# Optimization experiments

Hardware: AMD Instinct MI355X
Metric: run time of the kernel (lower is better)

The kernel has to match this reference:

```python
import jax, jax.numpy as jnp
import numpy as np

N = 100000      # nodes
E = 1600000     # edges
D_IN = 256
D_HID = 256
D_OUT = 256
DROP_P = 0.5


def setup_inputs() -> dict:
    key = jax.random.key(0)
    ks = jax.random.split(key, 10)
    s = 1.0 / np.sqrt(D_HID)
    return {
        "z": jax.random.normal(ks[0], (N, D_OUT), jnp.float32),
        "omega": jax.random.normal(ks[1], (N, D_IN), jnp.float32),
        "edge_index": jax.random.randint(ks[2], (2, E), 0, N, jnp.int32),
        "W_lin": jax.random.normal(ks[3], (D_IN, D_HID), jnp.float32) * s,
        "b_lin": jnp.zeros((D_HID,), jnp.float32),
        "W_g1": jax.random.normal(ks[4], (D_HID, D_HID), jnp.float32) * s,
        "b_g1": jnp.zeros((D_HID,), jnp.float32),
        "W_g2": jax.random.normal(ks[5], (D_HID, D_OUT), jnp.float32) * s,
        "b_g2": jnp.zeros((D_OUT,), jnp.float32),
        "mask1": jax.random.bernoulli(ks[6], 1.0 - DROP_P, (N, D_HID)),
        "mask2": jax.random.bernoulli(ks[7], 1.0 - DROP_P, (N, D_HID)),
    }


def _gcn_norm(edge_index):
    # add self-loops, symmetric normalization deg^-1/2 * deg^-1/2
    loop = jnp.arange(N, dtype=edge_index.dtype)
    src = jnp.concatenate([edge_index[0], loop])
    dst = jnp.concatenate([edge_index[1], loop])
    deg = jax.ops.segment_sum(jnp.ones_like(dst, jnp.float32), dst, num_segments=N)
    dinv = jax.lax.rsqrt(deg)  # deg >= 1 because of self-loops
    norm = dinv[src] * dinv[dst]  # [E+N]
    return src, dst, norm


def _gcn_conv(x, W, b, src, dst, norm):
    h = x @ W                                  # [N, d_out]
    msg = h[src] * norm[:, None]               # gather over edges
    out = jax.ops.segment_sum(msg, dst, num_segments=N)  # scatter-add
    return out + b


def _dropout(x, mask):
    return jnp.where(mask, x * (1.0 / (1.0 - DROP_P)), 0.0)


def reference(z, omega, edge_index, W_lin, b_lin, W_g1, b_g1, W_g2, b_g2, mask1, mask2):
    src, dst, norm = _gcn_norm(edge_index)
    # layer 0: Linear + relu + dropout
    h = _dropout(jax.nn.relu(omega @ W_lin + b_lin), mask1)
    # layer 1: GCNConv + relu + dropout
    h = _dropout(jax.nn.relu(_gcn_conv(h, W_g1, b_g1, src, dst, norm)), mask2)
    # layer 2: GCNConv
    h = _gcn_conv(h, W_g2, b_g2, src, dst, norm)
    return z * h
```

## Files before the change

### kernel.cpp

```cpp
#include <hip/hip_runtime.h>
#include <stdint.h>

#define NN 100000
#define EE 1600000
#define DD 256

typedef __bf16 bf16;
typedef __attribute__((ext_vector_type(8))) __bf16 bf16x8;
typedef __attribute__((ext_vector_type(4))) float f32x4;
typedef __attribute__((ext_vector_type(4))) unsigned int u32x4;
typedef __attribute__((ext_vector_type(8))) unsigned short u16x8;

typedef __attribute__((address_space(1))) const unsigned int g_u32c;
typedef __attribute__((address_space(3))) unsigned int lds_u32;

__device__ __forceinline__ float bflo(unsigned int u) {
    union { unsigned int u; float f; } x; x.u = u << 16; return x.f;
}
__device__ __forceinline__ float bfhi(unsigned int u) {
    union { unsigned int u; float f; } x; x.u = u & 0xFFFF0000u; return x.f;
}
__device__ __forceinline__ unsigned short f2bf(float f) {
    return __builtin_bit_cast(unsigned short, (__bf16)f);
}

#define NSUB 128
__global__ __launch_bounds__(256) void count_deg_k(
    const int* __restrict__ dst, int* __restrict__ cnt) {
    int bid = blockIdx.x;
    int prt = bid & 7;
    int sub = bid >> 3;
    int lo = prt * (NN >> 3);
    int hi = (prt == 7) ? NN : lo + (NN >> 3);
    const int per = EE / NSUB;
    int e0 = sub * per;
    int e1 = (sub == NSUB - 1) ? EE : e0 + per;
    for (int e = e0 + threadIdx.x; e < e1; e += 256) {
        int d = dst[e];
        if (d >= lo && d < hi) atomicAdd(&cnt[d], 1);
    }
}
__global__ __launch_bounds__(256) void scan_blk_k(const int* __restrict__ cnt,
                                                  int* __restrict__ part,
                                                  int* __restrict__ bsum,
                                                  float* __restrict__ dinv) {
    __shared__ int buf[256];
    int i = blockIdx.x * 256 + threadIdx.x;
    int v = 0;
    if (i < NN) { v = cnt[i] + 1; dinv[i] = rsqrtf((float)v); }
    buf[threadIdx.x] = v;
    __syncthreads();
    for (int off = 1; off < 256; off <<= 1) {
        int t = (threadIdx.x >= off) ? buf[threadIdx.x - off] : 0;
        __syncthreads();
        buf[threadIdx.x] += t;
        __syncthreads();
    }
    if (i < NN) part[i] = buf[threadIdx.x];
    if (threadIdx.x == 255) bsum[blockIdx.x] = buf[255];
}
__global__ __launch_bounds__(512) void scan_top_k(const int* __restrict__ bsum,
                                                  int* __restrict__ bpre, int nb) {
    __shared__ int buf[512];
    int v = (threadIdx.x < (unsigned)nb) ? bsum[threadIdx.x] : 0;
    buf[threadIdx.x] = v;
    __syncthreads();
    for (int off = 1; off < 512; off <<= 1) {
        int t = (threadIdx.x >= off) ? buf[threadIdx.x - off] : 0;
        __syncthreads();
        buf[threadIdx.x] += t;
        __syncthreads();
    }
    if (threadIdx.x < (unsigned)nb) bpre[threadIdx.x] = buf[threadIdx.x] - v;
}
__global__ void scan_fin_k(const int* __restrict__ part, const int* __restrict__ bpre,
                           const int* __restrict__ cnt,
                           int* __restrict__ offs, int* __restrict__ cur,
                           int* __restrict__ cs) {
    int i = blockIdx.x * 256 + threadIdx.x;
    if (i >= NN) return;
    int o1 = part[i] + bpre[blockIdx.x];
    offs[i + 1] = o1;
    if (i == 0) offs[0] = 0;
    int o = o1 - (cnt[i] + 1);
    cs[o] = i;
    cur[i] = o + 1;
}
__global__ __launch_bounds__(256) void fill_csr_k(
    const int* __restrict__ src, const int* __restrict__ dst,
    int* __restrict__ cur, int* __restrict__ cs) {
    int bid = blockIdx.x;
    int prt = bid & 7;
    int sub = bid >> 3;
    int lo = prt * (NN >> 3);
    int hi = (prt == 7) ? NN : lo + (NN >> 3);
    const int per = EE / NSUB;
    int e0 = sub * per;
    int e1 = (sub == NSUB - 1) ? EE : e0 + per;
    for (int e = e0 + threadIdx.x; e < e1; e += 256) {
        int d = dst[e];
        if (d >= lo && d < hi) {
            int s = src[e];
            int pos = atomicAdd(&cur[d], 1);
            cs[pos] = s;
        }
    }
}

__global__ __launch_bounds__(256) void prep_k(
    const float* __restrict__ W0, const float* __restrict__ W1, const float* __restrict__ W2,
    bf16* __restrict__ T0, bf16* __restrict__ T1, bf16* __restrict__ T2,
    const unsigned int* __restrict__ m, int* __restrict__ flag) {
    int b = blockIdx.x;
    if (b == 192) {
        if (threadIdx.x < 64) {
            unsigned int v = m[threadIdx.x];
            int bad = (v > 1u && v != 0x3F800000u) ? 1 : 0;
            unsigned long long bl = __ballot(bad);
            if (threadIdx.x == 0) *flag = (bl != 0ull) ? 1 : 0;
        }
        return;
    }
    const float* W = b < 64 ? W0 : (b < 128 ? W1 : W2);
    bf16*       T  = b < 64 ? T0 : (b < 128 ? T1 : T2);
    int bb = b & 63;
    __shared__ float tile[32][33];
    int bx = bb & 7, by = bb >> 3;
    int tx = threadIdx.x & 31, ty = threadIdx.x >> 5;
    #pragma unroll
    for (int r = 0; r < 32; r += 8)
        tile[ty + r][tx] = W[(size_t)(by * 32 + ty + r) * DD + bx * 32 + tx];
    __syncthreads();
    #pragma unroll
    for (int r = 0; r < 32; r += 8)
        T[(size_t)(bx * 32 + ty + r) * DD + by * 32 + tx] = (bf16)tile[tx][ty + r];
}

template <int ID, int EPI, int F32A>
__global__ __launch_bounds__(256) void gemm_k(
    const void* __restrict__ Ap, const bf16* __restrict__ Wt,
    const float* __restrict__ bias, const void* __restrict__ mask,
    const int* __restrict__ flagp, const float* __restrict__ z,
    const float* __restrict__ dinv, void* __restrict__ outp) {
    __shared__ __align__(16) bf16 As[64 * 64];
    __shared__ __align__(16) bf16 Bs[256 * 64];

    int m0 = blockIdx.x * 64;
    if (m0 >= NN) return;
    int tid = threadIdx.x;
    int wid = tid >> 6, lane = tid & 63;
    int lr = lane & 15, lk = lane >> 4;

    f32x4 acc[4][4] = {};

    for (int k0 = 0; k0 < DD; k0 += 64) {
        #pragma unroll
        for (int i = 0; i < 2; i++) {
            int f = i * 256 + tid;
            int row = f >> 3;
            int c   = (f & 7) * 8;
            int gr = m0 + row; if (gr > NN - 1) gr = NN - 1;
            if (F32A) {
                const float* sp = (const float*)Ap + (size_t)gr * DD + k0 + c;
                float4 v0 = *(const float4*)sp;
                float4 v1 = *(const float4*)(sp + 4);
                u16x8 o = { f2bf(v0.x), f2bf(v0.y), f2bf(v0.z), f2bf(v0.w),
                            f2bf(v1.x), f2bf(v1.y), f2bf(v1.z), f2bf(v1.w) };
                *(u16x8*)(As + row * 64 + c) = o;
            } else {
                __builtin_amdgcn_global_load_lds(
                    (g_u32c*)((const bf16*)Ap + (size_t)gr * DD + k0 + c),
                    (lds_u32*)(As + (size_t)f * 8), 16, 0, 0);
            }
        }
        #pragma unroll
        for (int i = 0; i < 8; i++) {
            int f = i * 256 + tid;
            int row = f >> 3;
            int c   = (f & 7) * 8;
            __builtin_amdgcn_global_load_lds(
                (g_u32c*)(Wt + (size_t)row * DD + k0 + c),
                (lds_u32*)(Bs + (size_t)f * 8), 16, 0, 0);
        }
        __syncthreads();
        #pragma unroll
        for (int kk = 0; kk < 2; kk++) {
            bf16x8 af[4], bfr[4];
            #pragma unroll
            for (int mi = 0; mi < 4; mi++)
                af[mi] = *(const bf16x8*)(As + (mi * 16 + lr) * 64 + kk * 32 + lk * 8);
            #pragma unroll
            for (int ni = 0; ni < 4; ni++)
                bfr[ni] = *(const bf16x8*)(Bs + (wid * 64 + ni * 16 + lr) * 64 + kk * 32 + lk * 8);
            #pragma unroll
            for (int mi = 0; mi < 4; mi++)
                #pragma unroll
                for (int ni = 0; ni < 4; ni++)
                    acc[mi][ni] = __builtin_amdgcn_mfma_f32_16x16x32_bf16(
                        bfr[ni], af[mi], acc[mi][ni], 0, 0, 0);
        }
        __syncthreads();
    }

    int bm = (EPI == 1) ? *flagp : 0;
    #pragma unroll
    for (int mi = 0; mi < 4; mi++) {
        int gr = m0 + mi * 16 + lr;
        if (gr >= NN) continue;
        float ds = (EPI == 1) ? dinv[gr] : 0.f;
        #pragma unroll
        for (int ni = 0; ni < 4; ni++) {
            int gc = wid * 64 + ni * 16 + lk * 4;
            size_t idx = (size_t)gr * DD + gc;
            float4 b4 = *(const float4*)(bias + gc);
            float v0 = acc[mi][ni][0] + b4.x;
            float v1 = acc[mi][ni][1] + b4.y;
            float v2 = acc[mi][ni][2] + b4.z;
            float v3 = acc[mi][ni][3] + b4.w;
            if (EPI == 1) {
                v0 = fmaxf(v0, 0.f); v1 = fmaxf(v1, 0.f);
                v2 = fmaxf(v2, 0.f); v3 = fmaxf(v3, 0.f);
                if (bm) {
                    uchar4 u = *(const uchar4*)((const unsigned char*)mask + idx);
                    v0 *= u.x ? 2.f : 0.f; v1 *= u.y ? 2.f : 0.f;
                    v2 *= u.z ? 2.f : 0.f; v3 *= u.w ? 2.f : 0.f;
                } else {
                    uint4 u = *(const uint4*)((const unsigned int*)mask + idx);
                    v0 *= u.x ? 2.f : 0.f; v1 *= u.y ? 2.f : 0.f;
                    v2 *= u.z ? 2.f : 0.f; v3 *= u.w ? 2.f : 0.f;
                }
                v0 *= ds; v1 *= ds; v2 *= ds; v3 *= ds;
                ushort4 o = { f2bf(v0), f2bf(v1), f2bf(v2), f2bf(v3) };
                *(ushort4*)((unsigned short*)outp + idx) = o;
            } else {
                f32x4 zz = __builtin_nontemporal_load((const f32x4*)(z + idx));
                f32x4 o = { v0 * zz.x, v1 * zz.y, v2 * zz.z, v3 * zz.w };
                __builtin_nontemporal_store(o, (f32x4*)((float*)outp + idx));
            }
        }
    }
}

#define AGG_GET(J, UVAR, MVAR)                                                   \
    {                                                                            \
        int _i = 2 * (J) + half;                                                 \
        int _s = __shfl(sl, _i & 63);                                            \
        MVAR = (_i < nume) ? 1.f : 0.f;                                          \
        UVAR = *(const u32x4*)(tb + (((size_t)(unsigned)_s) << 9) + lcoff);      \
    }
#define AGG_FMA(UVAR, MVAR)                                                      \
    {                                                                            \
        acc[0] = fmaf(MVAR, bflo(UVAR.x), acc[0]);                               \
        acc[1] = fmaf(MVAR, bfhi(UVAR.x), acc[1]);                               \
        acc[2] = fmaf(MVAR, bflo(UVAR.y), acc[2]);                               \
        acc[3] = fmaf(MVAR, bfhi(UVAR.y), acc[3]);                               \
        acc[4] = fmaf(MVAR, bflo(UVAR.z), acc[4]);                               \
        acc[5] = fmaf(MVAR, bfhi(UVAR.z), acc[5]);                               \
        acc[6] = fmaf(MVAR, bflo(UVAR.w), acc[6]);                               \
        acc[7] = fmaf(MVAR, bfhi(UVAR.w), acc[7]);                               \
    }

__global__ __launch_bounds__(256) void agg_k(
    const bf16* __restrict__ t, const int* __restrict__ offs,
    const int* __restrict__ cs, const float* __restrict__ dinv,
    bf16* __restrict__ out) {
    int node = blockIdx.x * 4 + (threadIdx.x >> 6);
    if (node >= NN) return;
    int lane = threadIdx.x & 63;
    int half = lane >> 5;
    int lc = lane & 31;
    int beg = offs[node], end = offs[node + 1];

    float acc[8] = {};
    const char* tb = (const char*)t;
    size_t lcoff = (size_t)(lc << 4);

    for (int base = beg; base < end; base += 64) {
        int nume = min(64, end - base);
        int sl = 0;
        if (lane < nume) sl = __builtin_nontemporal_load(cs + base + lane);
        int nit = (nume + 1) >> 1;

        u32x4 ua, ub, uc, ud;
        float ma, mb, mc, md;
        AGG_GET(0, ua, ma);
        AGG_GET(1, ub, mb);
        AGG_GET(2, uc, mc);
        int j = 0;
        for (; j + 3 < nit; j += 4) {
            AGG_GET(j + 3, ud, md); AGG_FMA(ua, ma);
            AGG_GET(j + 4, ua, ma); AGG_FMA(ub, mb);
            AGG_GET(j + 5, ub, mb); AGG_FMA(uc, mc);
            AGG_GET(j + 6, uc, mc); AGG_FMA(ud, md);
        }
        int rem = nit - j;
        if (rem > 0) AGG_FMA(ua, ma);
        if (rem > 1) AGG_FMA(ub, mb);
        if (rem > 2) AGG_FMA(uc, mc);
    }

    float dn = dinv[node];
    #pragma unroll
    for (int i = 0; i < 8; i++) {
        acc[i] += __shfl_xor(acc[i], 32);
        acc[i] *= dn;
    }
    if (half == 0) {
        u16x8 o = { f2bf(acc[0]), f2bf(acc[1]), f2bf(acc[2]), f2bf(acc[3]),
                    f2bf(acc[4]), f2bf(acc[5]), f2bf(acc[6]), f2bf(acc[7]) };
        __builtin_nontemporal_store(o, (u16x8*)((unsigned short*)out + (size_t)node * DD + lc * 8));
    }
}

extern "C" void kernel_launch(void* const* d_in, const int* in_sizes, int n_in,
                              void* d_out, int out_size, void* d_ws, size_t ws_size,
                              hipStream_t stream) {
    const float* z     = (const float*)d_in[0];
    const float* omega = (const float*)d_in[1];
    const int*   eidx  = (const int*)d_in[2];
    const float* W_lin = (const float*)d_in[3];
    const float* b_lin = (const float*)d_in[4];
    const float* W_g1  = (const float*)d_in[5];
    const float* b_g1  = (const float*)d_in[6];
    const float* W_g2  = (const float*)d_in[7];
    const float* b_g2  = (const float*)d_in[8];
    const void*  mask1 = d_in[9];
    const void*  mask2 = d_in[10];

    const int* e_src = eidx;
    const int* e_dst = eidx + EE;

    char* p = (char*)d_ws;
    size_t off = 0;
    auto alloc = [&](size_t bytes) -> char* {
        char* r = p + off;
        off = (off + bytes + 255) & ~(size_t)255;
        return r;
    };
    const int NB256 = (NN + 255) / 256;
    int*   flag = (int*)  alloc(4);
    int*   cnt  = (int*)  alloc((size_t)NN * 4);
    int*   offs = (int*)  alloc(((size_t)NN + 1) * 4);
    int*   cur  = (int*)  alloc((size_t)NN * 4);
    int*   part = (int*)  alloc((size_t)NN * 4);
    int*   bsum = (int*)  alloc(512 * 4);
    int*   bpre = (int*)  alloc(512 * 4);
    float* dinv = (float*)alloc((size_t)NN * 4);
    int*   cs   = (int*)  alloc((size_t)(EE + NN) * 4);
    bf16*  WtL  = (bf16*) alloc((size_t)DD * DD * 2);
    bf16*  Wt1  = (bf16*) alloc((size_t)DD * DD * 2);
    bf16*  Wt2  = (bf16*) alloc((size_t)DD * DD * 2);
    const size_t NBH = (size_t)NN * DD * 2;
    bf16*  S1   = (bf16*) alloc(NBH);
    bf16*  S2   = (bf16*) alloc(NBH);

    (void)hipMemsetAsync(cnt, 0, (size_t)NN * 4, stream);
    count_deg_k<<<NSUB * 8, 256, 0, stream>>>(e_dst, cnt);
    scan_blk_k <<<NB256, 256, 0, stream>>>(cnt, part, bsum, dinv);
    scan_top_k <<<1, 512, 0, stream>>>(bsum, bpre, NB256);
    scan_fin_k <<<NB256, 256, 0, stream>>>(part, bpre, cnt, offs, cur, cs);
    fill_csr_k <<<NSUB * 8, 256, 0, stream>>>(e_src, e_dst, cur, cs);

    prep_k<<<193, 256, 0, stream>>>(W_lin, W_g1, W_g2, WtL, Wt1, Wt2,
                                    (const unsigned int*)mask1, flag);

    const int GB = (NN + 63) / 64;
    gemm_k<0, 1, 1><<<GB, 256, 0, stream>>>(omega, WtL, b_lin, mask1, flag, nullptr, dinv, S1);
    agg_k<<<NN / 4, 256, 0, stream>>>(S1, offs, cs, dinv, S2);
    gemm_k<1, 1, 0><<<GB, 256, 0, stream>>>(S2, Wt1, b_g1, mask2, flag, nullptr, dinv, S1);
    agg_k<<<NN / 4, 256, 0, stream>>>(S1, offs, cs, dinv, S2);
    gemm_k<2, 2, 0><<<GB, 256, 0, stream>>>(S2, Wt2, b_g2, nullptr, flag, z, dinv, d_out);
}
```

Baseline: 611.3 us.

## Fuse neighbor aggregation into the following GEMM via shared-memory tile

Merges the sparse aggregation kernel with the next dense GEMM. Each block aggregates 64 nodes into an LDS tile and multiplies it by the weight matrix in two 128-column halves. This removes the bf16 round trip of the aggregated activations through global memory and two kernel launches. In exchange, each block serializes 16 nodes per wave during aggregation, so it exposes fewer concurrent gathers. The larger LDS footprint may also reduce occupancy.

```diff
diff --git a/kernel.cpp b/kernel.cpp
--- a/kernel.cpp
+++ b/kernel.cpp
@@ -136,12 +136,40 @@
         T[(size_t)(bx * 32 + ty + r) * DD + by * 32 + tx] = (bf16)tile[tx][ty + r];
 }
 
-template <int ID, int EPI, int F32A>
-__global__ __launch_bounds__(256) void gemm_k(
-    const void* __restrict__ Ap, const bf16* __restrict__ Wt,
+template <int EPI>
+__device__ __forceinline__ void epilogue4(
+    float v0, float v1, float v2, float v3, size_t idx, int gc,
+    const float* __restrict__ bias, const void* __restrict__ mask, int bm,
+    const float* __restrict__ z, float ds, void* __restrict__ outp) {
+    float4 b4 = *(const float4*)(bias + gc);
+    v0 += b4.x; v1 += b4.y; v2 += b4.z; v3 += b4.w;
+    if (EPI == 1) {
+        v0 = fmaxf(v0, 0.f); v1 = fmaxf(v1, 0.f);
+        v2 = fmaxf(v2, 0.f); v3 = fmaxf(v3, 0.f);
+        if (bm) {
+            uchar4 u = *(const uchar4*)((const unsigned char*)mask + idx);
+            v0 *= u.x ? 2.f : 0.f; v1 *= u.y ? 2.f : 0.f;
+            v2 *= u.z ? 2.f : 0.f; v3 *= u.w ? 2.f : 0.f;
+        } else {
+            uint4 u = *(const uint4*)((const unsigned int*)mask + idx);
+            v0 *= u.x ? 2.f : 0.f; v1 *= u.y ? 2.f : 0.f;
+            v2 *= u.z ? 2.f : 0.f; v3 *= u.w ? 2.f : 0.f;
+        }
+        v0 *= ds; v1 *= ds; v2 *= ds; v3 *= ds;
+        ushort4 o = { f2bf(v0), f2bf(v1), f2bf(v2), f2bf(v3) };
+        *(ushort4*)((unsigned short*)outp + idx) = o;
+    } else {
+        f32x4 zz = __builtin_nontemporal_load((const f32x4*)(z + idx));
+        f32x4 o = { v0 * zz.x, v1 * zz.y, v2 * zz.z, v3 * zz.w };
+        __builtin_nontemporal_store(o, (f32x4*)((float*)outp + idx));
+    }
+}
+
+__global__ __launch_bounds__(256) void gemm0_k(
+    const float* __restrict__ Ap, const bf16* __restrict__ Wt,
     const float* __restrict__ bias, const void* __restrict__ mask,
-    const int* __restrict__ flagp, const float* __restrict__ z,
-    const float* __restrict__ dinv, void* __restrict__ outp) {
+    const int* __restrict__ flagp, const float* __restrict__ dinv,
+    bf16* __restrict__ outp) {
     __shared__ __align__(16) bf16 As[64 * 64];
     __shared__ __align__(16) bf16 Bs[256 * 64];
 
@@ -160,18 +188,12 @@
             int row = f >> 3;
             int c   = (f & 7) * 8;
             int gr = m0 + row; if (gr > NN - 1) gr = NN - 1;
-            if (F32A) {
-                const float* sp = (const float*)Ap + (size_t)gr * DD + k0 + c;
-                float4 v0 = *(const float4*)sp;
-                float4 v1 = *(const float4*)(sp + 4);
-                u16x8 o = { f2bf(v0.x), f2bf(v0.y), f2bf(v0.z), f2bf(v0.w),
-                            f2bf(v1.x), f2bf(v1.y), f2bf(v1.z), f2bf(v1.w) };
-                *(u16x8*)(As + row * 64 + c) = o;
-            } else {
-                __builtin_amdgcn_global_load_lds(
-                    (g_u32c*)((const bf16*)Ap + (size_t)gr * DD + k0 + c),
-                    (lds_u32*)(As + (size_t)f * 8), 16, 0, 0);
-            }
+            const float* sp = Ap + (size_t)gr * DD + k0 + c;
+            float4 v0 = *(const float4*)sp;
+            float4 v1 = *(const float4*)(sp + 4);
+            u16x8 o = { f2bf(v0.x), f2bf(v0.y), f2bf(v0.z), f2bf(v0.w),
+                        f2bf(v1.x), f2bf(v1.y), f2bf(v1.z), f2bf(v1.w) };
+            *(u16x8*)(As + row * 64 + c) = o;
         }
         #pragma unroll
         for (int i = 0; i < 8; i++) {
@@ -202,41 +224,18 @@
         __syncthreads();
     }
 
-    int bm = (EPI == 1) ? *flagp : 0;
+    int bm = *flagp;
     #pragma unroll
     for (int mi = 0; mi < 4; mi++) {
         int gr = m0 + mi * 16 + lr;
         if (gr >= NN) continue;
-        float ds = (EPI == 1) ? dinv[gr] : 0.f;
+        float ds = dinv[gr];
         #pragma unroll
         for (int ni = 0; ni < 4; ni++) {
             int gc = wid * 64 + ni * 16 + lk * 4;
             size_t idx = (size_t)gr * DD + gc;
-            float4 b4 = *(const float4*)(bias + gc);
-            float v0 = acc[mi][ni][0] + b4.x;
-            float v1 = acc[mi][ni][1] + b4.y;
-            float v2 = acc[mi][ni][2] + b4.z;
-            float v3 = acc[mi][ni][3] + b4.w;
-            if (EPI == 1) {
-                v0 = fmaxf(v0, 0.f); v1 = fmaxf(v1, 0.f);
-                v2 = fmaxf(v2, 0.f); v3 = fmaxf(v3, 0.f);
-                if (bm) {
-                    uchar4 u = *(const uchar4*)((const unsigned char*)mask + idx);
-                    v0 *= u.x ? 2.f : 0.f; v1 *= u.y ? 2.f : 0.f;
-                    v2 *= u.z ? 2.f : 0.f; v3 *= u.w ? 2.f : 0.f;
-                } else {
-                    uint4 u = *(const uint4*)((const unsigned int*)mask + idx);
-                    v0 *= u.x ? 2.f : 0.f; v1 *= u.y ? 2.f : 0.f;
-                    v2 *= u.z ? 2.f : 0.f; v3 *= u.w ? 2.f : 0.f;
-                }
-                v0 *= ds; v1 *= ds; v2 *= ds; v3 *= ds;
-                ushort4 o = { f2bf(v0), f2bf(v1), f2bf(v2), f2bf(v3) };
-                *(ushort4*)((unsigned short*)outp + idx) = o;
-            } else {
-                f32x4 zz = __builtin_nontemporal_load((const f32x4*)(z + idx));
-                f32x4 o = { v0 * zz.x, v1 * zz.y, v2 * zz.z, v3 * zz.w };
-                __builtin_nontemporal_store(o, (f32x4*)((float*)outp + idx));
-            }
+            epilogue4<1>(acc[mi][ni][0], acc[mi][ni][1], acc[mi][ni][2], acc[mi][ni][3],
+                         idx, gc, bias, mask, bm, nullptr, ds, outp);
         }
     }
 }
@@ -260,55 +259,111 @@
         acc[7] = fmaf(MVAR, bfhi(UVAR.w), acc[7]);                               \
     }
 
-__global__ __launch_bounds__(256) void agg_k(
-    const bf16* __restrict__ t, const int* __restrict__ offs,
+template <int ID, int EPI>
+__global__ __launch_bounds__(256) void aggemm_k(
+    const bf16* __restrict__ S, const int* __restrict__ offs,
     const int* __restrict__ cs, const float* __restrict__ dinv,
-    bf16* __restrict__ out) {
-    int node = blockIdx.x * 4 + (threadIdx.x >> 6);
-    if (node >= NN) return;
-    int lane = threadIdx.x & 63;
-    int half = lane >> 5;
-    int lc = lane & 31;
-    int beg = offs[node], end = offs[node + 1];
-
-    float acc[8] = {};
-    const char* tb = (const char*)t;
+    const bf16* __restrict__ Wt, const float* __restrict__ bias,
+    const void* __restrict__ mask, const int* __restrict__ flagp,
+    const float* __restrict__ z, void* __restrict__ outp) {
+    __shared__ __align__(16) bf16 Ag[64][264];
+    __shared__ __align__(16) bf16 Bs[128 * 64];
+
+    int m0 = blockIdx.x * 64;
+    int tid = threadIdx.x;
+    int wid = tid >> 6, lane = tid & 63;
+    int half = lane >> 5, lc = lane & 31;
+    int lr = lane & 15, lk = lane >> 4;
+    const char* tb = (const char*)S;
     size_t lcoff = (size_t)(lc << 4);
 
-    for (int base = beg; base < end; base += 64) {
-        int nume = min(64, end - base);
-        int sl = 0;
-        if (lane < nume) sl = __builtin_nontemporal_load(cs + base + lane);
-        int nit = (nume + 1) >> 1;
-
-        u32x4 ua, ub, uc, ud;
-        float ma, mb, mc, md;
-        AGG_GET(0, ua, ma);
-        AGG_GET(1, ub, mb);
-        AGG_GET(2, uc, mc);
-        int j = 0;
-        for (; j + 3 < nit; j += 4) {
-            AGG_GET(j + 3, ud, md); AGG_FMA(ua, ma);
-            AGG_GET(j + 4, ua, ma); AGG_FMA(ub, mb);
-            AGG_GET(j + 5, ub, mb); AGG_FMA(uc, mc);
-            AGG_GET(j + 6, uc, mc); AGG_FMA(ud, md);
-        }
-        int rem = nit - j;
-        if (rem > 0) AGG_FMA(ua, ma);
-        if (rem > 1) AGG_FMA(ub, mb);
-        if (rem > 2) AGG_FMA(uc, mc);
-    }
-
-    float dn = dinv[node];
+    for (int nn = 0; nn < 16; nn++) {
+        int node = m0 + wid * 16 + nn;
+        if (node >= NN) break;
+        int beg = offs[node], end = offs[node + 1];
+        float acc[8] = {};
+        for (int base = beg; base < end; base += 64) {
+            int nume = min(64, end - base);
+            int sl = 0;
+            if (lane < nume) sl = __builtin_nontemporal_load(cs + base + lane);
+            int nit = (nume + 1) >> 1;
+            u32x4 ua, ub, uc, ud;
+            float ma, mb, mc, md;
+            AGG_GET(0, ua, ma);
+            AGG_GET(1, ub, mb);
+            AGG_GET(2, uc, mc);
+            int j = 0;
+            for (; j + 3 < nit; j += 4) {
+                AGG_GET(j + 3, ud, md); AGG_FMA(ua, ma);
+                AGG_GET(j + 4, ua, ma); AGG_FMA(ub, mb);
+                AGG_GET(j + 5, ub, mb); AGG_FMA(uc, mc);
+                AGG_GET(j + 6, uc, mc); AGG_FMA(ud, md);
+            }
+            int rem = nit - j;
+            if (rem > 0) AGG_FMA(ua, ma);
+            if (rem > 1) AGG_FMA(ub, mb);
+            if (rem > 2) AGG_FMA(uc, mc);
+        }
+        float dn = dinv[node];
+        #pragma unroll
+        for (int i = 0; i < 8; i++) {
+            acc[i] += __shfl_xor(acc[i], 32);
+            acc[i] *= dn;
+        }
+        if (half == 0) {
+            u16x8 o = { f2bf(acc[0]), f2bf(acc[1]), f2bf(acc[2]), f2bf(acc[3]),
+                        f2bf(acc[4]), f2bf(acc[5]), f2bf(acc[6]), f2bf(acc[7]) };
+            *(u16x8*)(&Ag[wid * 16 + nn][lc * 8]) = o;
+        }
+    }
+    __syncthreads();
+
+    int bm = (EPI == 1) ? *flagp : 0;
     #pragma unroll
-    for (int i = 0; i < 8; i++) {
-        acc[i] += __shfl_xor(acc[i], 32);
-        acc[i] *= dn;
-    }
-    if (half == 0) {
-        u16x8 o = { f2bf(acc[0]), f2bf(acc[1]), f2bf(acc[2]), f2bf(acc[3]),
-                    f2bf(acc[4]), f2bf(acc[5]), f2bf(acc[6]), f2bf(acc[7]) };
-        __builtin_nontemporal_store(o, (u16x8*)((unsigned short*)out + (size_t)node * DD + lc * 8));
+    for (int h = 0; h < 2; h++) {
+        f32x4 acc[4][2] = {};
+        for (int k0 = 0; k0 < DD; k0 += 64) {
+            #pragma unroll
+            for (int i = 0; i < 4; i++) {
+                int f = i * 256 + tid;
+                int row = f >> 3;
+                int c   = (f & 7) * 8;
+                __builtin_amdgcn_global_load_lds(
+                    (g_u32c*)(Wt + (size_t)(h * 128 + row) * DD + k0 + c),
+                    (lds_u32*)(Bs + (size_t)f * 8), 16, 0, 0);
+            }
+            __syncthreads();
+            #pragma unroll
+            for (int kk = 0; kk < 2; kk++) {
+                bf16x8 af[4], bfr[2];
+                #pragma unroll
+                for (int mi = 0; mi < 4; mi++)
+                    af[mi] = *(const bf16x8*)(&Ag[mi * 16 + lr][k0 + kk * 32 + lk * 8]);
+                #pragma unroll
+                for (int ni = 0; ni < 2; ni++)
+                    bfr[ni] = *(const bf16x8*)(Bs + (wid * 32 + ni * 16 + lr) * 64 + kk * 32 + lk * 8);
+                #pragma unroll
+                for (int mi = 0; mi < 4; mi++)
+                    #pragma unroll
+                    for (int ni = 0; ni < 2; ni++)
+                        acc[mi][ni] = __builtin_amdgcn_mfma_f32_16x16x32_bf16(
+                            bfr[ni], af[mi], acc[mi][ni], 0, 0, 0);
+            }
+            __syncthreads();
+        }
+        #pragma unroll
+        for (int mi = 0; mi < 4; mi++) {
+            int gr = m0 + mi * 16 + lr;
+            if (gr >= NN) continue;
+            float ds = (EPI == 1) ? dinv[gr] : 0.f;
+            #pragma unroll
+            for (int ni = 0; ni < 2; ni++) {
+                int gc = h * 128 + wid * 32 + ni * 16 + lk * 4;
+                size_t idx = (size_t)gr * DD + gc;
+                epilogue4<EPI>(acc[mi][ni][0], acc[mi][ni][1], acc[mi][ni][2], acc[mi][ni][3],
+                               idx, gc, bias, mask, bm, z, ds, outp);
+            }
+        }
     }
 }
 
@@ -365,9 +420,9 @@
                                     (const unsigned int*)mask1, flag);
 
     const int GB = (NN + 63) / 64;
-    gemm_k<0, 1, 1><<<GB, 256, 0, stream>>>(omega, WtL, b_lin, mask1, flag, nullptr, dinv, S1);
-    agg_k<<<NN / 4, 256, 0, stream>>>(S1, offs, cs, dinv, S2);
-    gemm_k<1, 1, 0><<<GB, 256, 0, stream>>>(S2, Wt1, b_g1, mask2, flag, nullptr, dinv, S1);
-    agg_k<<<NN / 4, 256, 0, stream>>>(S1, offs, cs, dinv, S2);
-    gemm_k<2, 2, 0><<<GB, 256, 0, stream>>>(S2, Wt2, b_g2, nullptr, flag, z, dinv, d_out);
-}
+    gemm0_k<<<GB, 256, 0, stream>>>(omega, WtL, b_lin, mask1, flag, dinv, S1);
+    aggemm_k<1, 1><<<GB, 256, 0, stream>>>(S1, offs, cs, dinv, Wt1, b_g1,
+                                           mask2, flag, nullptr, S2);
+    aggemm_k<2, 2><<<GB, 256, 0, stream>>>(S2, offs, cs, dinv, Wt2, b_g2,
+                                           nullptr, flag, z, d_out);
+}
```

Result: slower. 652.5 us (+6.7%).
